# Kernel optimization log

Hardware: AMD Instinct MI355X
Metric: run time of the kernel (lower is better)

The kernel has to match this reference:

```python
import jax, jax.numpy as jnp
import numpy as np

B, D, H, W = 2, 256, 64, 64
NH = 4
EPS = 1e-5


def _ln(x, g, b):
    # LayerNorm over channel dim of NCHW tensor (matches permute->LN(C)->permute)
    mu = jnp.mean(x, axis=1, keepdims=True)
    var = jnp.mean((x - mu) ** 2, axis=1, keepdims=True)
    xn = (x - mu) * jax.lax.rsqrt(var + EPS)
    return xn * g[None, :, None, None] + b[None, :, None, None]


def _conv1x1(x, w, b):
    # w: (out_c, in_c)
    return jnp.einsum('bchw,oc->bohw', x, w) + b[None, :, None, None]


def _dwconv3x3(x, w, b):
    # depthwise 3x3, w: (C, 1, 3, 3)
    y = jax.lax.conv_general_dilated(
        x, w, window_strides=(1, 1), padding='SAME',
        dimension_numbers=('NCHW', 'OIHW', 'NCHW'), feature_group_count=D)
    return y + b[None, :, None, None]


def setup_inputs() -> dict:
    key = jax.random.key(0)
    ks = jax.random.split(key, 12)
    sc = 0.02

    def n(k, shape):
        return jax.random.normal(k, shape, dtype=jnp.float32) * sc

    return {
        'image_embedding': jax.random.normal(ks[0], (B, D, H, W), dtype=jnp.float32),
        'guide': jax.random.normal(ks[1], (B, D, H, W), dtype=jnp.float32),
        'ln1_g': jnp.ones((D,), jnp.float32), 'ln1_b': jnp.zeros((D,), jnp.float32),
        'ln2_g': jnp.ones((D,), jnp.float32), 'ln2_b': jnp.zeros((D,), jnp.float32),
        'qw1': n(ks[2], (D, D)), 'qb1': jnp.zeros((D,), jnp.float32),
        'qw2': n(ks[3], (D, 1, 3, 3)), 'qb2': jnp.zeros((D,), jnp.float32),
        'kw1': n(ks[4], (D, D)), 'kb1': jnp.zeros((D,), jnp.float32),
        'kw2': n(ks[5], (D, 1, 3, 3)), 'kb2': jnp.zeros((D,), jnp.float32),
        'vw1': n(ks[6], (D, D)), 'vb1': jnp.zeros((D,), jnp.float32),
        'vw2': n(ks[7], (D, 1, 3, 3)), 'vb2': jnp.zeros((D,), jnp.float32),
        'ow': n(ks[8], (D, D)), 'ob': jnp.zeros((D,), jnp.float32),
    }


def reference(image_embedding, guide, ln1_g, ln1_b, ln2_g, ln2_b,
              qw1, qb1, qw2, qb2, kw1, kb1, kw2, kb2,
              vw1, vb1, vw2, vb2, ow, ob):
    residual = image_embedding
    x = _ln(image_embedding, ln1_g, ln1_b)
    g = _ln(guide, ln2_g, ln2_b)

    q = _dwconv3x3(_conv1x1(x, qw1, qb1), qw2, qb2)
    k = _dwconv3x3(_conv1x1(g, kw1, kb1), kw2, kb2)
    v = _dwconv3x3(_conv1x1(g, vw1, vb1), vw2, vb2)

    hd = D // NH
    scale = hd ** -0.5

    def to_heads(t):  # (B,C,H,W) -> (B, NH, HW, hd)
        return t.reshape(B, NH, hd, H * W).transpose(0, 1, 3, 2)

    q = to_heads(q) * scale
    k = to_heads(k)
    v = to_heads(v)

    attn = jax.nn.softmax(jnp.einsum('bhnd,bhmd->bhnm', q, k), axis=-1)
    out = jnp.einsum('bhnm,bhmd->bhnd', attn, v)
    out = out.transpose(0, 1, 3, 2).reshape(B, D, H, W)
    out = _conv1x1(out, ow, ob)
    return residual + out
```

## Files before the change

kernel.cpp:

```cpp
#include <hip/hip_runtime.h>
#include <cstdint>
#include <cstddef>

typedef unsigned short u16;
typedef unsigned int u32;
typedef __attribute__((ext_vector_type(8))) short short8;
typedef __attribute__((ext_vector_type(4))) float f32x4;
typedef __attribute__((ext_vector_type(16))) float f32x16;
typedef __attribute__((ext_vector_type(2))) unsigned int u32x2;

#define CD 256
#define HWD 4096
#define NHD 4
#define HDD 64

static __device__ __forceinline__ u16 f2b(float f) {
    u32 u = __builtin_bit_cast(u32, f);
    return (u16)((u + 0x7fffu + ((u >> 16) & 1u)) >> 16);
}
static __device__ __forceinline__ float b2f(u16 h) {
    return __builtin_bit_cast(float, (u32)h << 16);
}
static __device__ __forceinline__ u32 pk2(float a, float b) {
    return (u32)f2b(a) | ((u32)f2b(b) << 16);
}
static __device__ __forceinline__ float fexp2(float x) {
#if __has_builtin(__builtin_amdgcn_exp2f)
    return __builtin_amdgcn_exp2f(x);
#else
    return __expf(x * 0.69314718056f);
#endif
}
static __device__ __forceinline__ u32 cvtpk(float lo, float hi) {
    u32 r;
    asm("v_cvt_pk_bf16_f32 %0, %1, %2" : "=v"(r) : "v"(lo), "v"(hi));
    return r;
}
static __device__ __forceinline__ u32x2 plswap(u32 a, u32 b) {
    return __builtin_amdgcn_permlane32_swap(a, b, false, false);
}
static __device__ __forceinline__ void async16(const void* g, void* l) {
    __builtin_amdgcn_global_load_lds(
        (const __attribute__((address_space(1))) unsigned int*)g,
        (__attribute__((address_space(3))) unsigned int*)l,
        16, 0, 0);
}

__global__ __launch_bounds__(256) void ln_transpose(
    const float* __restrict__ x0, const float* __restrict__ x1,
    const float* __restrict__ g0, const float* __restrict__ b0,
    const float* __restrict__ g1, const float* __restrict__ b1,
    u16* __restrict__ out0, u16* __restrict__ out1)
{
    int bid = blockIdx.x;
    int t = bid >> 8, b = (bid >> 7) & 1, p0 = (bid & 127) << 5;
    const float* x = t ? x1 : x0;
    const float* g = t ? g1 : g0;
    const float* bb = t ? b1 : b0;
    u16* out = t ? out1 : out0;

    int tid = threadIdx.x;
    int tx = tid & 31, ty = tid >> 5;
    const float* xb = x + (size_t)b * CD * HWD + p0 + tx;

    __shared__ float red[2][8][32];
    __shared__ u16 T[256][33];

    float s = 0.f, sq = 0.f;
    #pragma unroll 8
    for (int i = 0; i < 32; ++i) {
        float v = xb[(size_t)(ty * 32 + i) * HWD];
        s += v; sq += v * v;
    }
    red[0][ty][tx] = s; red[1][ty][tx] = sq;
    __syncthreads();
    float st = 0.f, sqt = 0.f;
    #pragma unroll
    for (int j = 0; j < 8; ++j) { st += red[0][j][tx]; sqt += red[1][j][tx]; }
    float mean = st * (1.f / 256.f);
    float var = sqt * (1.f / 256.f) - mean * mean;
    float rstd = rsqrtf(var + 1e-5f);

    #pragma unroll 8
    for (int i = 0; i < 32; ++i) {
        int c = ty * 32 + i;
        float v = (xb[(size_t)c * HWD] - mean) * rstd * g[c] + bb[c];
        T[c][tx] = f2b(v);
    }
    __syncthreads();

    #pragma unroll
    for (int pass = 0; pass < 4; ++pass) {
        int idx = pass * 256 + tid;
        int p = idx >> 5, cs = (idx & 31) * 8;
        u16 tmp[8];
        #pragma unroll
        for (int j = 0; j < 8; ++j) tmp[j] = T[cs + j][p];
        *(uint4*)&out[((size_t)b * HWD + p0 + p) * CD + cs] = *(const uint4*)tmp;
    }
}

__global__ __launch_bounds__(256) void qkv_gemm(
    const u16* __restrict__ xT, const u16* __restrict__ gT,
    const float* __restrict__ qw1, const float* __restrict__ qb1,
    const float* __restrict__ kw1, const float* __restrict__ kb1,
    const float* __restrict__ vw1, const float* __restrict__ vb1,
    u16* __restrict__ q1, u16* __restrict__ k1, u16* __restrict__ v1)
{
    int z = blockIdx.z;
    int mm = z >> 1, b = z & 1;
    const u16* X    = (mm == 0) ? xT : gT;
    const float* W  = (mm == 0) ? qw1 : (mm == 1) ? kw1 : vw1;
    const float* Bi = (mm == 0) ? qb1 : (mm == 1) ? kb1 : vb1;
    u16* Y          = (mm == 0) ? q1 : (mm == 1) ? k1 : v1;

    int n0 = blockIdx.x * 128;
    int p0 = blockIdx.y * 64;

    __shared__ u16 As[64][40];
    __shared__ u16 Bs[128][40];

    int tid = threadIdx.x;
    int lane = tid & 63, w = tid >> 6;
    int wm = w >> 1, wn = w & 1;
    int l15 = lane & 15, quad = lane >> 4;

    f32x4 acc[2][4];
    #pragma unroll
    for (int mi = 0; mi < 2; ++mi)
        #pragma unroll
        for (int nj = 0; nj < 4; ++nj)
            acc[mi][nj] = (f32x4){0.f, 0.f, 0.f, 0.f};

    const u16* Xb = X + (size_t)b * HWD * CD;

    int arow = tid >> 2, aseg = (tid & 3) * 8;
    const u16* agp = Xb + (size_t)(p0 + arow) * CD + aseg;
    int brow = tid >> 1, bkh = (tid & 1) * 16;
    const float* wgp = W + (size_t)(n0 + brow) * CD + bkh;

    uint4 ra = *(const uint4*)(agp);
    float4 rw0 = ((const float4*)wgp)[0], rw1 = ((const float4*)wgp)[1];
    float4 rw2 = ((const float4*)wgp)[2], rw3 = ((const float4*)wgp)[3];

    for (int kt = 0; kt < 8; ++kt) {
        __syncthreads();
        *(uint4*)&As[arow][aseg] = ra;
        {
            uint4 qa, qb;
            qa.x = pk2(rw0.x, rw0.y); qa.y = pk2(rw0.z, rw0.w);
            qa.z = pk2(rw1.x, rw1.y); qa.w = pk2(rw1.z, rw1.w);
            qb.x = pk2(rw2.x, rw2.y); qb.y = pk2(rw2.z, rw2.w);
            qb.z = pk2(rw3.x, rw3.y); qb.w = pk2(rw3.z, rw3.w);
            *(uint4*)&Bs[brow][bkh] = qa;
            *(uint4*)&Bs[brow][bkh + 8] = qb;
        }
        if (kt < 7) {
            ra = *(const uint4*)(agp + (kt + 1) * 32);
            const float* wg2 = wgp + (kt + 1) * 32;
            rw0 = ((const float4*)wg2)[0]; rw1 = ((const float4*)wg2)[1];
            rw2 = ((const float4*)wg2)[2]; rw3 = ((const float4*)wg2)[3];
        }
        __syncthreads();

        short8 af[2], bf[4];
        #pragma unroll
        for (int mi = 0; mi < 2; ++mi)
            af[mi] = *(const short8*)&As[wm * 32 + mi * 16 + l15][quad * 8];
        #pragma unroll
        for (int nj = 0; nj < 4; ++nj)
            bf[nj] = *(const short8*)&Bs[wn * 64 + nj * 16 + l15][quad * 8];
        #pragma unroll
        for (int mi = 0; mi < 2; ++mi)
            #pragma unroll
            for (int nj = 0; nj < 4; ++nj)
                acc[mi][nj] = __builtin_amdgcn_mfma_f32_16x16x32_bf16(
                    af[mi], bf[nj], acc[mi][nj], 0, 0, 0);
    }

    u16* Yb = Y + (size_t)b * HWD * CD;
    float bias[4];
    #pragma unroll
    for (int nj = 0; nj < 4; ++nj)
        bias[nj] = Bi[n0 + wn * 64 + nj * 16 + l15];
    #pragma unroll
    for (int mi = 0; mi < 2; ++mi) {
        #pragma unroll
        for (int r = 0; r < 4; ++r) {
            int p = p0 + wm * 32 + mi * 16 + quad * 4 + r;
            #pragma unroll
            for (int nj = 0; nj < 4; ++nj) {
                int ch = n0 + wn * 64 + nj * 16 + l15;
                Yb[(size_t)p * CD + ch] = f2b(acc[mi][nj][r] + bias[nj]);
            }
        }
    }
}

__global__ __launch_bounds__(256) void dwconv_nc(
    const u16* __restrict__ q1, const u16* __restrict__ k1, const u16* __restrict__ v1,
    const float* __restrict__ qw2, const float* __restrict__ qb2,
    const float* __restrict__ kw2, const float* __restrict__ kb2,
    const float* __restrict__ vw2, const float* __restrict__ vb2,
    u16* __restrict__ Q, u16* __restrict__ K, u16* __restrict__ Vt)
{
    int bid = blockIdx.x;
    int which = bid >> 9;
    int b = (bid >> 8) & 1;
    int p0 = (bid & 255) * 16;

    const u16* in = ((which == 0) ? q1 : (which == 1) ? k1 : v1) + (size_t)b * HWD * CD;
    const float* wsrc = (which == 0) ? qw2 : (which == 1) ? kw2 : vw2;
    const float* bsrc = (which == 0) ? qb2 : (which == 1) ? kb2 : vb2;
    float oscale = (which == 0) ? 0.18033688011112042f : 1.0f;

    int c = threadIdx.x;
    float w9[9];
    #pragma unroll
    for (int j = 0; j < 9; ++j) w9[j] = wsrc[c * 9 + j];
    float bias = bsrc[c];

    int h = p0 >> 6, w0 = p0 & 63;

    float accv[16];
    #pragma unroll
    for (int pi = 0; pi < 16; ++pi) accv[pi] = bias;

    #pragma unroll
    for (int dh = 0; dh < 3; ++dh) {
        int hh = h + dh - 1;
        if (hh < 0 || hh >= 64) continue;
        const u16* rp = in + ((size_t)hh * 64) * CD + c;
        float r[18];
        r[0] = (w0 > 0) ? b2f(rp[(size_t)(w0 - 1) * CD]) : 0.f;
        #pragma unroll
        for (int j = 1; j <= 16; ++j)
            r[j] = b2f(rp[(size_t)(w0 - 1 + j) * CD]);
        r[17] = (w0 < 48) ? b2f(rp[(size_t)(w0 + 16) * CD]) : 0.f;

        float wa = w9[dh * 3 + 0], wb = w9[dh * 3 + 1], wc = w9[dh * 3 + 2];
        #pragma unroll
        for (int pi = 0; pi < 16; ++pi)
            accv[pi] += wa * r[pi] + wb * r[pi + 1] + wc * r[pi + 2];
    }

    if (which == 2) {
        u32 w8[8];
        #pragma unroll
        for (int j = 0; j < 8; ++j) w8[j] = pk2(accv[2 * j], accv[2 * j + 1]);
        uint4* dst = (uint4*)(Vt + ((size_t)(b * CD + c)) * HWD + p0);
        dst[0] = make_uint4(w8[0], w8[1], w8[2], w8[3]);
        dst[1] = make_uint4(w8[4], w8[5], w8[6], w8[7]);
    } else {
        u16* out = ((which == 0) ? Q : K) + (size_t)b * HWD * CD;
        #pragma unroll
        for (int pi = 0; pi < 16; ++pi)
            out[(size_t)(p0 + pi) * CD + c] = f2b(accv[pi] * oscale);
    }
}

__global__ __launch_bounds__(256, 4) void attn_kernel(
    const u16* __restrict__ Q, const u16* __restrict__ K,
    const u16* __restrict__ Vt, u16* __restrict__ Opart,
    float* __restrict__ Psum)
{
    int qt = blockIdx.x;
    int bh = blockIdx.y;
    int ks = blockIdx.z;
    int b = bh >> 2, nh = bh & 3;

    __shared__ u16 Ks_[2][64 * 64];
    __shared__ u16 Vs_[2][64 * 64];

    int tid = threadIdx.x;
    int lane = tid & 63, w = tid >> 6;
    int l31 = lane & 31, h = lane >> 5;
    int sw = l31 & 7;

    const u16* Qb = Q + ((size_t)b * HWD) * CD + nh * 64;
    const u16* Kb = K + ((size_t)b * HWD) * CD + nh * 64;
    const u16* Vb = Vt + ((size_t)bh * HDD) * HWD;

    int q0 = qt * 128 + w * 32;

    short8 qf[4];
    #pragma unroll
    for (int si = 0; si < 4; ++si)
        qf[si] = *(const short8*)(Qb + (size_t)(q0 + l31) * CD + si * 16 + h * 8);

    int rr = lane >> 3;
    int gseg = (lane & 7) ^ rr;
    const u16* kgb = Kb + (size_t)(ks * 1024 + w * 16 + rr) * CD + gseg * 8;
    const u16* vgb = Vb + (size_t)(w * 16 + rr) * HWD + ks * 1024 + gseg * 8;

    f32x16 acc[2];
    #pragma unroll
    for (int db = 0; db < 2; ++db)
        #pragma unroll
        for (int r = 0; r < 16; ++r) acc[db][r] = 0.f;
    float psum = 0.f;

    #pragma unroll
    for (int j = 0; j < 2; ++j) {
        async16(kgb + (size_t)(j * 8) * CD, &Ks_[0][(w * 16 + j * 8) * 64]);
        async16(vgb + (size_t)(j * 8) * HWD, &Vs_[0][(w * 16 + j * 8) * 64]);
    }

    for (int it = 0; it < 16; ++it) {
        int cur = it & 1;
        __syncthreads();
        if (it + 1 < 16) {
            int nxt = cur ^ 1;
            #pragma unroll
            for (int j = 0; j < 2; ++j) {
                async16(kgb + (size_t)((it + 1) * 64 + j * 8) * CD,
                        &Ks_[nxt][(w * 16 + j * 8) * 64]);
                async16(vgb + (size_t)(j * 8) * HWD + (it + 1) * 64,
                        &Vs_[nxt][(w * 16 + j * 8) * 64]);
            }
        }

        #pragma unroll
        for (int kb = 0; kb < 2; ++kb) {
            short8 kf[4];
            #pragma unroll
            for (int si = 0; si < 4; ++si)
                kf[si] = *(const short8*)&Ks_[cur][(kb * 32 + l31) * 64 +
                                                   (((si * 2 + h) ^ sw) << 3)];
            f32x16 st;
            #pragma unroll
            for (int r = 0; r < 16; ++r) st[r] = 0.f;
            #pragma unroll
            for (int si = 0; si < 4; ++si)
                st = __builtin_amdgcn_mfma_f32_32x32x16_bf16(
                    kf[si], qf[si], st, 0, 0, 0);

            float e[16];
            #pragma unroll
            for (int r = 0; r < 16; ++r) e[r] = fexp2(st[r]);
            #pragma unroll
            for (int r = 0; r < 16; r += 4)
                psum += (e[r] + e[r + 1]) + (e[r + 2] + e[r + 3]);

            u32 wv[8];
            #pragma unroll
            for (int m = 0; m < 8; ++m) wv[m] = cvtpk(e[2 * m], e[2 * m + 1]);
            u32x2 s02 = plswap(wv[0], wv[2]);
            u32x2 s13 = plswap(wv[1], wv[3]);
            u32x2 s46 = plswap(wv[4], wv[6]);
            u32x2 s57 = plswap(wv[5], wv[7]);
            union { u32 u[4]; short8 s8; } p0_, p1_;
            p0_.u[0] = s02.x; p0_.u[1] = s13.x; p0_.u[2] = s02.y; p0_.u[3] = s13.y;
            p1_.u[0] = s46.x; p1_.u[1] = s57.x; p1_.u[2] = s46.y; p1_.u[3] = s57.y;

            #pragma unroll
            for (int db = 0; db < 2; ++db) {
                short8 vf0 = *(const short8*)&Vs_[cur][(db * 32 + l31) * 64 +
                                 ((((kb * 2 + 0) * 2 + h) ^ sw) << 3)];
                acc[db] = __builtin_amdgcn_mfma_f32_32x32x16_bf16(
                    p0_.s8, vf0, acc[db], 0, 0, 0);
                short8 vf1 = *(const short8*)&Vs_[cur][(db * 32 + l31) * 64 +
                                 ((((kb * 2 + 1) * 2 + h) ^ sw) << 3)];
                acc[db] = __builtin_amdgcn_mfma_f32_32x32x16_bf16(
                    p1_.s8, vf1, acc[db], 0, 0, 0);
            }
        }
    }

    u16* Ob = Opart + (((size_t)ks * 8 + bh) * HWD) * HDD;
    #pragma unroll
    for (int db = 0; db < 2; ++db)
        #pragma unroll
        for (int r = 0; r < 16; ++r) {
            int n = q0 + (r & 3) + 8 * (r >> 2) + 4 * h;
            Ob[(size_t)n * HDD + db * 32 + l31] = f2b(acc[db][r]);
        }

    float s = psum + __shfl_xor(psum, 32);
    float* Pb = Psum + ((size_t)ks * 8 + bh) * HWD + q0;
    if (lane < 32) Pb[lane] = s;
}

__global__ __launch_bounds__(256) void out_gemm(
    const float* __restrict__ W, const float* __restrict__ Bi,
    const u16* __restrict__ Opart, const float* __restrict__ Psum,
    const float* __restrict__ residual, float* __restrict__ out)
{
    int b = blockIdx.z;
    int m0 = blockIdx.y * 64;
    int n0 = blockIdx.x * 64;

    __shared__ u16 As[64][40];
    __shared__ u16 Bs[64][40];

    int tid = threadIdx.x;
    int lane = tid & 63, w = tid >> 6;
    int wm = w >> 1, wn = w & 1;
    int l15 = lane & 15, quad = lane >> 4;

    f32x4 acc[2][2];
    #pragma unroll
    for (int mi = 0; mi < 2; ++mi)
        #pragma unroll
        for (int nj = 0; nj < 2; ++nj)
            acc[mi][nj] = (f32x4){0.f, 0.f, 0.f, 0.f};

    int arow = tid >> 2, aseg = (tid & 3) * 8;
    const float* wgp = W + (size_t)(m0 + arow) * CD + aseg;
    int brow = tid >> 2, bseg = (tid & 3) * 8;
    int pn = n0 + brow;

    float4 rw0 = ((const float4*)wgp)[0], rw1 = ((const float4*)wgp)[1];

    uint4 ro[4]; float rinv;
    {
        int c = bseg;
        int bh = b * 4 + (c >> 6), d0 = c & 63;
        float p = 0.f;
        #pragma unroll
        for (int s = 0; s < 4; ++s) {
            ro[s] = *(const uint4*)&Opart[(((size_t)s * 8 + bh) * HWD + pn) * HDD + d0];
            p += Psum[((size_t)s * 8 + bh) * HWD + pn];
        }
        rinv = 1.f / p;
    }

    for (int kt = 0; kt < 8; ++kt) {
        __syncthreads();
        {
            uint4 qa;
            qa.x = pk2(rw0.x, rw0.y); qa.y = pk2(rw0.z, rw0.w);
            qa.z = pk2(rw1.x, rw1.y); qa.w = pk2(rw1.z, rw1.w);
            *(uint4*)&As[arow][aseg] = qa;
        }
        {
            float v[8];
            #pragma unroll
            for (int j = 0; j < 8; ++j) v[j] = 0.f;
            #pragma unroll
            for (int s = 0; s < 4; ++s) {
                u16 t[8];
                *(uint4*)t = ro[s];
                #pragma unroll
                for (int j = 0; j < 8; ++j) v[j] += b2f(t[j]);
            }
            uint4 bb;
            bb.x = pk2(v[0] * rinv, v[1] * rinv);
            bb.y = pk2(v[2] * rinv, v[3] * rinv);
            bb.z = pk2(v[4] * rinv, v[5] * rinv);
            bb.w = pk2(v[6] * rinv, v[7] * rinv);
            *(uint4*)&Bs[brow][bseg] = bb;
        }
        if (kt < 7) {
            const float* wg2 = wgp + (kt + 1) * 32;
            rw0 = ((const float4*)wg2)[0]; rw1 = ((const float4*)wg2)[1];
            int c = (kt + 1) * 32 + bseg;
            int bh = b * 4 + (c >> 6), d0 = c & 63;
            float p = 0.f;
            #pragma unroll
            for (int s = 0; s < 4; ++s) {
                ro[s] = *(const uint4*)&Opart[(((size_t)s * 8 + bh) * HWD + pn) * HDD + d0];
                p += Psum[((size_t)s * 8 + bh) * HWD + pn];
            }
            rinv = 1.f / p;
        }
        __syncthreads();

        short8 af[2], bf[2];
        #pragma unroll
        for (int mi = 0; mi < 2; ++mi)
            af[mi] = *(const short8*)&As[wm * 32 + mi * 16 + l15][quad * 8];
        #pragma unroll
        for (int nj = 0; nj < 2; ++nj)
            bf[nj] = *(const short8*)&Bs[wn * 32 + nj * 16 + l15][quad * 8];
        #pragma unroll
        for (int mi = 0; mi < 2; ++mi)
            #pragma unroll
            for (int nj = 0; nj < 2; ++nj)
                acc[mi][nj] = __builtin_amdgcn_mfma_f32_16x16x32_bf16(
                    af[mi], bf[nj], acc[mi][nj], 0, 0, 0);
    }

    #pragma unroll
    for (int mi = 0; mi < 2; ++mi) {
        int mb = m0 + wm * 32 + mi * 16 + quad * 4;
        #pragma unroll
        for (int r = 0; r < 4; ++r) {
            float bias = Bi[mb + r];
            const float* res = residual + (size_t)(b * CD + mb + r) * HWD;
            float* o = out + (size_t)(b * CD + mb + r) * HWD;
            #pragma unroll
            for (int nj = 0; nj < 2; ++nj) {
                int n = n0 + wn * 32 + nj * 16 + l15;
                o[n] = acc[mi][nj][r] + bias + res[n];
            }
        }
    }
}

extern "C" void kernel_launch(void* const* d_in, const int* in_sizes, int n_in,
                              void* d_out, int out_size, void* d_ws, size_t ws_size,
                              hipStream_t stream) {
    (void)in_sizes; (void)n_in; (void)out_size; (void)ws_size;

    const float* image = (const float*)d_in[0];
    const float* guide = (const float*)d_in[1];
    const float* ln1_g = (const float*)d_in[2];
    const float* ln1_b = (const float*)d_in[3];
    const float* ln2_g = (const float*)d_in[4];
    const float* ln2_b = (const float*)d_in[5];
    const float* qw1 = (const float*)d_in[6];
    const float* qb1 = (const float*)d_in[7];
    const float* qw2 = (const float*)d_in[8];
    const float* qb2 = (const float*)d_in[9];
    const float* kw1 = (const float*)d_in[10];
    const float* kb1 = (const float*)d_in[11];
    const float* kw2 = (const float*)d_in[12];
    const float* kb2 = (const float*)d_in[13];
    const float* vw1 = (const float*)d_in[14];
    const float* vb1 = (const float*)d_in[15];
    const float* vw2 = (const float*)d_in[16];
    const float* vb2 = (const float*)d_in[17];
    const float* ow  = (const float*)d_in[18];
    const float* ob  = (const float*)d_in[19];
    float* out = (float*)d_out;

    char* ws = (char*)d_ws;
    u16* xT    = (u16*)(ws + (size_t)0  * (1 << 20));
    u16* gT    = (u16*)(ws + (size_t)4  * (1 << 20));
    u16* q1    = (u16*)(ws + (size_t)8  * (1 << 20));
    u16* k1    = (u16*)(ws + (size_t)12 * (1 << 20));
    u16* v1    = (u16*)(ws + (size_t)16 * (1 << 20));
    u16* Qh    = (u16*)(ws + (size_t)20 * (1 << 20));
    u16* Kh    = (u16*)(ws + (size_t)24 * (1 << 20));
    u16* Vt    = (u16*)(ws + (size_t)28 * (1 << 20));
    u16*   Opart = (u16*)(ws + (size_t)0  * (1 << 20));
    float* Psum  = (float*)(ws + (size_t)18 * (1 << 20));

    ln_transpose<<<dim3(512), dim3(256), 0, stream>>>(
        image, guide, ln1_g, ln1_b, ln2_g, ln2_b, xT, gT);

    qkv_gemm<<<dim3(2, 64, 6), dim3(256), 0, stream>>>(
        xT, gT, qw1, qb1, kw1, kb1, vw1, vb1, q1, k1, v1);

    dwconv_nc<<<dim3(1536), dim3(256), 0, stream>>>(
        q1, k1, v1, qw2, qb2, kw2, kb2, vw2, vb2, Qh, Kh, Vt);

    attn_kernel<<<dim3(32, 8, 4), dim3(256), 0, stream>>>(Qh, Kh, Vt, Opart, Psum);

    out_gemm<<<dim3(64, 4, 2), dim3(256), 0, stream>>>(
        ow, ob, Opart, Psum, image, out);
}
```

Before: 185.9 us.

## Double attention key splits and read V directly from global memory

The attention kernel now splits the key dimension into 8 chunks instead of 4, so twice as many blocks are launched and each processes half as many key tiles. V tiles are no longer staged through shared memory; each lane loads its MFMA fragments directly from global memory, which frees LDS and allows a higher occupancy hint. The output GEMM reduces over 8 partial outputs, and the workspace buffers are moved to avoid overlap. The risks are uncoalesced, unpipelined global V loads on the critical path and more partial-sum traffic in the reduction.

```diff
diff --git a/kernel.cpp b/kernel.cpp
--- a/kernel.cpp
+++ b/kernel.cpp
@@ -13,6 +13,7 @@
 #define HWD 4096
 #define NHD 4
 #define HDD 64
+#define NSPLIT 8
 
 static __device__ __forceinline__ u16 f2b(float f) {
     u32 u = __builtin_bit_cast(u32, f);
@@ -259,7 +260,7 @@
     }
 }
 
-__global__ __launch_bounds__(256, 4) void attn_kernel(
+__global__ __launch_bounds__(256, 6) void attn_kernel(
     const u16* __restrict__ Q, const u16* __restrict__ K,
     const u16* __restrict__ Vt, u16* __restrict__ Opart,
     float* __restrict__ Psum)
@@ -270,7 +271,6 @@
     int b = bh >> 2, nh = bh & 3;
 
     __shared__ u16 Ks_[2][64 * 64];
-    __shared__ u16 Vs_[2][64 * 64];
 
     int tid = threadIdx.x;
     int lane = tid & 63, w = tid >> 6;
@@ -290,8 +290,10 @@
 
     int rr = lane >> 3;
     int gseg = (lane & 7) ^ rr;
-    const u16* kgb = Kb + (size_t)(ks * 1024 + w * 16 + rr) * CD + gseg * 8;
-    const u16* vgb = Vb + (size_t)(w * 16 + rr) * HWD + ks * 1024 + gseg * 8;
+    const u16* kgb = Kb + (size_t)(ks * 512 + w * 16 + rr) * CD + gseg * 8;
+
+    const u16* vp0 = Vb + (size_t)(l31) * HWD + ks * 512;
+    const u16* vp1 = Vb + (size_t)(32 + l31) * HWD + ks * 512;
 
     f32x16 acc[2];
     #pragma unroll
@@ -301,27 +303,29 @@
     float psum = 0.f;
 
     #pragma unroll
-    for (int j = 0; j < 2; ++j) {
+    for (int j = 0; j < 2; ++j)
         async16(kgb + (size_t)(j * 8) * CD, &Ks_[0][(w * 16 + j * 8) * 64]);
-        async16(vgb + (size_t)(j * 8) * HWD, &Vs_[0][(w * 16 + j * 8) * 64]);
-    }
-
-    for (int it = 0; it < 16; ++it) {
+
+    for (int it = 0; it < 8; ++it) {
         int cur = it & 1;
         __syncthreads();
-        if (it + 1 < 16) {
+        if (it + 1 < 8) {
             int nxt = cur ^ 1;
             #pragma unroll
-            for (int j = 0; j < 2; ++j) {
+            for (int j = 0; j < 2; ++j)
                 async16(kgb + (size_t)((it + 1) * 64 + j * 8) * CD,
                         &Ks_[nxt][(w * 16 + j * 8) * 64]);
-                async16(vgb + (size_t)(j * 8) * HWD + (it + 1) * 64,
-                        &Vs_[nxt][(w * 16 + j * 8) * 64]);
-            }
         }
 
         #pragma unroll
         for (int kb = 0; kb < 2; ++kb) {
+            const u16* v0 = vp0 + it * 64 + kb * 32;
+            const u16* v1 = vp1 + it * 64 + kb * 32;
+            short8 vf00 = *(const short8*)(v0 + h * 8);
+            short8 vf01 = *(const short8*)(v0 + 16 + h * 8);
+            short8 vf10 = *(const short8*)(v1 + h * 8);
+            short8 vf11 = *(const short8*)(v1 + 16 + h * 8);
+
             short8 kf[4];
             #pragma unroll
             for (int si = 0; si < 4; ++si)
@@ -353,17 +357,10 @@
             p0_.u[0] = s02.x; p0_.u[1] = s13.x; p0_.u[2] = s02.y; p0_.u[3] = s13.y;
             p1_.u[0] = s46.x; p1_.u[1] = s57.x; p1_.u[2] = s46.y; p1_.u[3] = s57.y;
 
-            #pragma unroll
-            for (int db = 0; db < 2; ++db) {
-                short8 vf0 = *(const short8*)&Vs_[cur][(db * 32 + l31) * 64 +
-                                 ((((kb * 2 + 0) * 2 + h) ^ sw) << 3)];
-                acc[db] = __builtin_amdgcn_mfma_f32_32x32x16_bf16(
-                    p0_.s8, vf0, acc[db], 0, 0, 0);
-                short8 vf1 = *(const short8*)&Vs_[cur][(db * 32 + l31) * 64 +
-                                 ((((kb * 2 + 1) * 2 + h) ^ sw) << 3)];
-                acc[db] = __builtin_amdgcn_mfma_f32_32x32x16_bf16(
-                    p1_.s8, vf1, acc[db], 0, 0, 0);
-            }
+            acc[0] = __builtin_amdgcn_mfma_f32_32x32x16_bf16(p0_.s8, vf00, acc[0], 0, 0, 0);
+            acc[0] = __builtin_amdgcn_mfma_f32_32x32x16_bf16(p1_.s8, vf01, acc[0], 0, 0, 0);
+            acc[1] = __builtin_amdgcn_mfma_f32_32x32x16_bf16(p0_.s8, vf10, acc[1], 0, 0, 0);
+            acc[1] = __builtin_amdgcn_mfma_f32_32x32x16_bf16(p1_.s8, vf11, acc[1], 0, 0, 0);
         }
     }
 
@@ -412,13 +409,13 @@
 
     float4 rw0 = ((const float4*)wgp)[0], rw1 = ((const float4*)wgp)[1];
 
-    uint4 ro[4]; float rinv;
+    uint4 ro[NSPLIT]; float rinv;
     {
         int c = bseg;
         int bh = b * 4 + (c >> 6), d0 = c & 63;
         float p = 0.f;
         #pragma unroll
-        for (int s = 0; s < 4; ++s) {
+        for (int s = 0; s < NSPLIT; ++s) {
             ro[s] = *(const uint4*)&Opart[(((size_t)s * 8 + bh) * HWD + pn) * HDD + d0];
             p += Psum[((size_t)s * 8 + bh) * HWD + pn];
         }
@@ -438,7 +435,7 @@
             #pragma unroll
             for (int j = 0; j < 8; ++j) v[j] = 0.f;
             #pragma unroll
-            for (int s = 0; s < 4; ++s) {
+            for (int s = 0; s < NSPLIT; ++s) {
                 u16 t[8];
                 *(uint4*)t = ro[s];
                 #pragma unroll
@@ -458,7 +455,7 @@
             int bh = b * 4 + (c >> 6), d0 = c & 63;
             float p = 0.f;
             #pragma unroll
-            for (int s = 0; s < 4; ++s) {
+            for (int s = 0; s < NSPLIT; ++s) {
                 ro[s] = *(const uint4*)&Opart[(((size_t)s * 8 + bh) * HWD + pn) * HDD + d0];
                 p += Psum[((size_t)s * 8 + bh) * HWD + pn];
             }
@@ -534,8 +531,8 @@
     u16* Qh    = (u16*)(ws + (size_t)20 * (1 << 20));
     u16* Kh    = (u16*)(ws + (size_t)24 * (1 << 20));
     u16* Vt    = (u16*)(ws + (size_t)28 * (1 << 20));
-    u16*   Opart = (u16*)(ws + (size_t)0  * (1 << 20));
-    float* Psum  = (float*)(ws + (size_t)18 * (1 << 20));
+    u16*   Opart = (u16*)(ws + (size_t)40 * (1 << 20));
+    float* Psum  = (float*)(ws + (size_t)72 * (1 << 20));
 
     ln_transpose<<<dim3(512), dim3(256), 0, stream>>>(
         image, guide, ln1_g, ln1_b, ln2_g, ln2_b, xT, gT);
@@ -546,7 +543,7 @@
     dwconv_nc<<<dim3(1536), dim3(256), 0, stream>>>(
         q1, k1, v1, qw2, qb2, kw2, kb2, vw2, vb2, Qh, Kh, Vt);
 
-    attn_kernel<<<dim3(32, 8, 4), dim3(256), 0, stream>>>(Qh, Kh, Vt, Opart, Psum);
+    attn_kernel<<<dim3(32, 8, NSPLIT), dim3(256), 0, stream>>>(Qh, Kh, Vt, Opart, Psum);
 
     out_gemm<<<dim3(64, 4, 2), dim3(256), 0, stream>>>(
         ow, ob, Opart, Psum, image, out);
```

After: 309.6 us. 66.5% more time.
